# Kernel optimization log

Hardware: AMD Instinct MI355X
Metric: run time of the kernel (lower is better)

The kernel has to match this reference:

```python
import jax, jax.numpy as jnp
import numpy as np

EMBED = 64
HEAD = 16

def setup_inputs() -> dict:
    key = jax.random.key(0)
    k1, k2, k3, k4 = jax.random.split(key, 4)
    x = jax.random.normal(k1, (4, 4096, EMBED), dtype=jnp.float32)
    # store weights as [in, out] so forward is x @ W (equivalent to torch Linear with W.T)
    Wq = jax.random.normal(k2, (EMBED, HEAD), dtype=jnp.float32) * (1.0 / np.sqrt(EMBED))
    Wk = jax.random.normal(k3, (EMBED, HEAD), dtype=jnp.float32) * (1.0 / np.sqrt(EMBED))
    Wv = jax.random.normal(k4, (EMBED, EMBED), dtype=jnp.float32) * (1.0 / np.sqrt(EMBED))
    return {"x": x, "Wq": Wq, "Wk": Wk, "Wv": Wv}

def reference(x, Wq, Wk, Wv):
    # q,k: [B,T,HEAD]; v: [B,T,EMBED]
    q = x @ Wq
    k = x @ Wk
    v = x @ Wv
    scores = jnp.einsum('bqh,bkh->bqk', q, k)  # [B,T,T]
    T = scores.shape[-1]
    # causal mask: positions with key > query set to -inf BEFORE scaling (matches original; same result)
    causal = jnp.tril(jnp.ones((T, T), dtype=bool))
    scores = jnp.where(causal, scores, -jnp.inf)
    attn = jax.nn.softmax(scores / np.sqrt(HEAD).astype(np.float32), axis=-1)
    return jnp.einsum('bqk,bkd->bqd', attn, v)  # [B,T,EMBED]
```

## Files before the change

kernel.cpp:

```cpp
#include <hip/hip_runtime.h>


#define TSEQ 4096
#define NBATCH 4
#define MFIX 24.0f

typedef __attribute__((ext_vector_type(4)))  float fvec4;
typedef __attribute__((ext_vector_type(16))) float f32x16;
typedef __attribute__((ext_vector_type(8)))  short s16x8;

union I4S8 { int i[4]; s16x8 v; };

static __device__ __forceinline__ unsigned short f2bf(float f) {
    unsigned u = __float_as_uint(f);
    u += 0x7FFFu + ((u >> 16) & 1u);
    return (unsigned short)(u >> 16);
}

static __device__ __forceinline__ int cvt_pk_bf16(float lo, float hi) {
    int r;
    asm("v_cvt_pk_bf16_f32 %0, %1, %2" : "=v"(r) : "v"(lo), "v"(hi));
    return r;
}

__global__ __launch_bounds__(256, 2) void proj_kernel(
    const float* __restrict__ x,  const float* __restrict__ Wq,
    const float* __restrict__ Wk, const float* __restrict__ Wv,
    unsigned short* __restrict__ qb, unsigned short* __restrict__ kb,
    unsigned short* __restrict__ vf)
{
    __shared__ __align__(16) unsigned short Wh[96][72], Wl[96][72];
    const int tid  = threadIdx.x;
    const int w    = tid >> 6;
    const int lane = tid & 63;
    const int col  = lane & 31;
    const int g    = lane >> 5;

    const float SCQ = 0.25f * 1.44269504088896340736f;
    #pragma unroll
    for (int j = 0; j < 4; ++j) {
        const int idx = tid + 256 * j;
        const int n = idx & 15, k = idx >> 4;
        float wv = Wq[idx] * SCQ;
        unsigned short h = f2bf(wv);
        Wh[n][k] = h;
        Wl[n][k] = f2bf(wv - __uint_as_float((unsigned)h << 16));
    }
    #pragma unroll
    for (int j = 0; j < 4; ++j) {
        const int idx = tid + 256 * j;
        const int n = idx & 15, k = idx >> 4;
        float wv = Wk[idx];
        unsigned short h = f2bf(wv);
        Wh[16 + n][k] = h;
        Wl[16 + n][k] = f2bf(wv - __uint_as_float((unsigned)h << 16));
    }
    #pragma unroll
    for (int j = 0; j < 16; ++j) {
        const int idx = tid + 256 * j;
        const int n = idx & 63, k = idx >> 6;
        float wv = Wv[idx];
        unsigned short h = f2bf(wv);
        Wh[32 + n][k] = h;
        Wl[32 + n][k] = f2bf(wv - __uint_as_float((unsigned)h << 16));
    }
    __syncthreads();

    const int row0 = blockIdx.x * 128 + w * 32;
    const int arow = row0 + col;

    s16x8 xh[4], xl[4];
    #pragma unroll
    for (int kc = 0; kc < 4; ++kc) {
        const float* xp = x + (size_t)arow * 64 + kc * 16 + 8 * g;
        fvec4 xa = *(const fvec4*)(xp);
        fvec4 xb = *(const fvec4*)(xp + 4);
        I4S8 uh, ul;
        uh.i[0] = cvt_pk_bf16(xa[0], xa[1]);
        uh.i[1] = cvt_pk_bf16(xa[2], xa[3]);
        uh.i[2] = cvt_pk_bf16(xb[0], xb[1]);
        uh.i[3] = cvt_pk_bf16(xb[2], xb[3]);
        float l0 = xa[0] - __uint_as_float((unsigned)uh.i[0] << 16);
        float l1 = xa[1] - __uint_as_float((unsigned)uh.i[0] & 0xffff0000u);
        float l2 = xa[2] - __uint_as_float((unsigned)uh.i[1] << 16);
        float l3 = xa[3] - __uint_as_float((unsigned)uh.i[1] & 0xffff0000u);
        float l4 = xb[0] - __uint_as_float((unsigned)uh.i[2] << 16);
        float l5 = xb[1] - __uint_as_float((unsigned)uh.i[2] & 0xffff0000u);
        float l6 = xb[2] - __uint_as_float((unsigned)uh.i[3] << 16);
        float l7 = xb[3] - __uint_as_float((unsigned)uh.i[3] & 0xffff0000u);
        ul.i[0] = cvt_pk_bf16(l0, l1);
        ul.i[1] = cvt_pk_bf16(l2, l3);
        ul.i[2] = cvt_pk_bf16(l4, l5);
        ul.i[3] = cvt_pk_bf16(l6, l7);
        xh[kc] = uh.v; xl[kc] = ul.v;
    }

    f32x16 acc0 = (f32x16)0.0f, acc1 = (f32x16)0.0f, acc2 = (f32x16)0.0f;
    #pragma unroll
    for (int nt = 0; nt < 3; ++nt) {
        const int n = nt * 32 + col;
        f32x16 a = nt == 0 ? acc0 : (nt == 1 ? acc1 : acc2);
        #pragma unroll
        for (int kc = 0; kc < 4; ++kc) {
            s16x8 bh = *(const s16x8*)&Wh[n][kc * 16 + 8 * g];
            s16x8 bl = *(const s16x8*)&Wl[n][kc * 16 + 8 * g];
            a = __builtin_amdgcn_mfma_f32_32x32x16_bf16(xh[kc], bh, a, 0, 0, 0);
            a = __builtin_amdgcn_mfma_f32_32x32x16_bf16(xl[kc], bh, a, 0, 0, 0);
            a = __builtin_amdgcn_mfma_f32_32x32x16_bf16(xh[kc], bl, a, 0, 0, 0);
        }
        if (nt == 0) acc0 = a; else if (nt == 1) acc1 = a; else acc2 = a;
    }

    {
        unsigned short* dst = (col < 16) ? (qb + col) : (kb + (col - 16));
        #pragma unroll
        for (int rr = 0; rr < 16; ++rr) {
            const int grow = row0 + (rr & 3) + 8 * (rr >> 2) + 4 * g;
            dst[(size_t)grow * 16] = f2bf(acc0[rr]);
        }
    }
    {
        const int tile = row0 >> 6;
        const int hw   = (row0 >> 5) & 1;
        unsigned short* const vtile = vf + (size_t)tile * 4096;
        #pragma unroll
        for (int mt = 0; mt < 2; ++mt) {
            const f32x16 a = mt ? acc2 : acc1;
            #pragma unroll
            for (int ci = 0; ci < 2; ++ci) {
                I4S8 pk;
                pk.i[0] = cvt_pk_bf16(a[8*ci + 0], a[8*ci + 1]);
                pk.i[1] = cvt_pk_bf16(a[8*ci + 2], a[8*ci + 3]);
                pk.i[2] = cvt_pk_bf16(a[8*ci + 4], a[8*ci + 5]);
                pk.i[3] = cvt_pk_bf16(a[8*ci + 6], a[8*ci + 7]);
                const int c = 2 * hw + ci;
                *(s16x8*)(vtile + ((c * 2 + mt) * 64 + lane) * 8) = pk.v;
            }
        }
    }
}

template<int MODE>
static __device__ __forceinline__ void do_tile(
    const unsigned short* kp, const unsigned short* vtile, const int lane,
    const s16x8 qf, const int col, const int g,
    f32x16& o0, f32x16& o1, float& lsum)
{
    const int NC = (MODE == 1) ? 2 : 4;
    s16x8 kf0 = *(const s16x8*)(kp);
    s16x8 kf1;
    if (MODE != 1) kf1 = *(const s16x8*)(kp + 512);
    s16x8 va[4][2];
    #pragma unroll
    for (int c = 0; c < NC; ++c) {
        va[c][0] = *(const s16x8*)(vtile + ((c * 2 + 0) * 64 + lane) * 8);
        va[c][1] = *(const s16x8*)(vtile + ((c * 2 + 1) * 64 + lane) * 8);
    }
    f32x16 s0 = __builtin_amdgcn_mfma_f32_32x32x16_bf16(kf0, qf, (f32x16)0.0f, 0, 0, 0);
    f32x16 s1;
    if (MODE != 1) s1 = __builtin_amdgcn_mfma_f32_32x32x16_bf16(kf1, qf, (f32x16)0.0f, 0, 0, 0);

    int pw[16];
    float psA = 0.f, psB = 0.f, psC = 0.f, psD = 0.f;
    #pragma unroll
    for (int rr = 0; rr < 16; ++rr) {
        float ev = __builtin_amdgcn_exp2f(s0[rr] - MFIX);
        if (MODE == 1) {
            const int drow = (rr & 3) + 8 * (rr >> 2) + 4 * g;
            ev = (drow <= col) ? ev : 0.f;
        }
        s0[rr] = ev;
        if ((rr & 3) == 0) psA += ev; else if ((rr & 3) == 1) psB += ev;
        else if ((rr & 3) == 2) psC += ev; else psD += ev;
    }
    #pragma unroll
    for (int j = 0; j < 8; ++j) pw[j] = cvt_pk_bf16(s0[2*j], s0[2*j+1]);
    if (MODE != 1) {
        #pragma unroll
        for (int rr = 0; rr < 16; ++rr) {
            float ev = __builtin_amdgcn_exp2f(s1[rr] - MFIX);
            if (MODE == 2) {
                const int drow = (rr & 3) + 8 * (rr >> 2) + 4 * g;
                ev = (drow <= col) ? ev : 0.f;
            }
            s1[rr] = ev;
            if ((rr & 3) == 0) psA += ev; else if ((rr & 3) == 1) psB += ev;
            else if ((rr & 3) == 2) psC += ev; else psD += ev;
        }
        #pragma unroll
        for (int j = 0; j < 8; ++j) pw[8 + j] = cvt_pk_bf16(s1[2*j], s1[2*j+1]);
    }
    lsum += (psA + psB) + (psC + psD);

    #pragma unroll
    for (int mt = 0; mt < 2; ++mt) {
        f32x16 oacc = mt ? o1 : o0;
        #pragma unroll
        for (int c = 0; c < NC; ++c) {
            I4S8 pu;
            pu.i[0] = pw[4 * c + 0]; pu.i[1] = pw[4 * c + 1];
            pu.i[2] = pw[4 * c + 2]; pu.i[3] = pw[4 * c + 3];
            oacc = __builtin_amdgcn_mfma_f32_32x32x16_bf16(va[c][mt], pu.v, oacc, 0, 0, 0);
        }
        if (mt) o1 = oacc; else o0 = oacc;
    }
}

__global__ __launch_bounds__(1024, 4) void attn_kernel(
    const unsigned short* __restrict__ qb, const unsigned short* __restrict__ kb,
    const unsigned short* __restrict__ vf, float* __restrict__ out)
{
    __shared__ float pl[16][32];
    __shared__ __align__(16) float pO[2048][18];
    __shared__ float outS[32][66];

    const int tid  = threadIdx.x;
    const int w    = tid >> 6;
    const int lane = tid & 63;
    const int col  = lane & 31;
    const int g    = lane >> 5;
    const int b    = blockIdx.y;
    const int p    = blockIdx.x;

    const unsigned short* const kbase = kb + (size_t)b * TSEQ * 16;
    const unsigned short* const vbase = vf + (size_t)b * 64 * 4096;

    for (int half = 0; half < 2; ++half) {
        const int i  = half ? (127 - p) : p;
        const int q0 = i * 32;
        const int n  = (i + 2) >> 1;

        const s16x8 qf = *(const s16x8*)(qb + ((size_t)(b * TSEQ) + q0 + col) * 16 + 8 * g);

        f32x16 o0 = (f32x16)0.0f, o1 = (f32x16)0.0f;
        float lsum = 0.f;

        int kt = w;
        for (; kt + 1 < n; kt += 16) {
            do_tile<0>(kbase + ((size_t)((kt << 6) + col)) * 16 + 8 * g,
                       vbase + (size_t)kt * 4096, lane, qf, col, g, o0, o1, lsum);
        }
        if (kt == n - 1) {
            const unsigned short* kp = kbase + ((size_t)((kt << 6) + col)) * 16 + 8 * g;
            const unsigned short* vtile = vbase + (size_t)kt * 4096;
            if (i & 1) do_tile<2>(kp, vtile, lane, qf, col, g, o0, o1, lsum);
            else       do_tile<1>(kp, vtile, lane, qf, col, g, o0, o1, lsum);
        }
        lsum += __shfl_xor(lsum, 32);

        if (g == 0) pl[w][col] = lsum;
        #pragma unroll
        for (int mt = 0; mt < 2; ++mt) {
            const f32x16 oa = mt ? o1 : o0;
            #pragma unroll
            for (int rr = 0; rr < 16; ++rr) {
                const int dv = mt * 32 + (rr & 3) + 8 * (rr >> 2) + 4 * g;
                pO[dv * 32 + col][w] = oa[rr];
            }
        }
        __syncthreads();

        {
            const int q   = tid & 31;
            const int dvh = tid >> 5;
            float L = 0.f;
            #pragma unroll
            for (int ww = 0; ww < 16; ++ww) L += pl[ww][q];
            const float inv = 1.0f / L;
            #pragma unroll
            for (int pass = 0; pass < 2; ++pass) {
                const int dv = dvh + 32 * pass;
                const float* prow = pO[dv * 32 + q];
                float s = 0.f;
                #pragma unroll
                for (int c = 0; c < 8; ++c) {
                    float2 v2 = *(const float2*)(prow + 2 * c);
                    s += v2.x + v2.y;
                }
                outS[q][dv] = s * inv;
            }
        }
        __syncthreads();

        {
            const int q2  = tid >> 5;
            const int dvp = (tid & 31) * 2;
            float2 v2 = *(const float2*)&outS[q2][dvp];
            *(float2*)(out + ((size_t)(b * TSEQ) + q0 + q2) * 64 + dvp) = v2;
        }
    }
}

extern "C" void kernel_launch(void* const* d_in, const int* in_sizes, int n_in,
                              void* d_out, int out_size, void* d_ws, size_t ws_size,
                              hipStream_t stream) {
    const float* x  = (const float*)d_in[0];
    const float* Wq = (const float*)d_in[1];
    const float* Wk = (const float*)d_in[2];
    const float* Wv = (const float*)d_in[3];

    unsigned short* qb = (unsigned short*)d_ws;
    unsigned short* kb = qb + (size_t)NBATCH * TSEQ * 16;
    unsigned short* vf = kb + (size_t)NBATCH * TSEQ * 16;
    float* out = (float*)d_out;

    proj_kernel<<<dim3((NBATCH * TSEQ) / 128), 256, 0, stream>>>(x, Wq, Wk, Wv, qb, kb, vf);
    attn_kernel<<<dim3(64, NBATCH), 1024, 0, stream>>>(qb, kb, vf, out);
}
```

Before: 27.49 us.

## Prefetch K across tiles, interleave PV MFMAs, restage x via LDS, shrink proj blocks

The attention inner loop now loads the next tile's K fragments one iteration ahead and issues each half's PV MFMAs right after its softmax, wrapping MFMA groups in s_setprio. The fixed exp2 offset MFIX is dropped, and pO padding changes from 18 to 17 floats. The projection kernel uses 128-thread blocks over 64 rows and stages x through LDS. Together these aim to hide load latency and cut register pressure and bank conflicts. Removing the offset risks exp2 overflow if scores grow large.

After: 36.34 us. +32.2%, slower.

```diff
diff --git a/kernel.cpp b/kernel.cpp
--- a/kernel.cpp
+++ b/kernel.cpp
@@ -3,10 +3,10 @@
 
 #define TSEQ 4096
 #define NBATCH 4
-#define MFIX 24.0f
 
 typedef __attribute__((ext_vector_type(4)))  float fvec4;
 typedef __attribute__((ext_vector_type(16))) float f32x16;
+typedef __attribute__((ext_vector_type(4)))  short s16x4;
 typedef __attribute__((ext_vector_type(8)))  short s16x8;
 
 union I4S8 { int i[4]; s16x8 v; };
@@ -23,23 +23,39 @@
     return r;
 }
 
-__global__ __launch_bounds__(256, 2) void proj_kernel(
+static __device__ __forceinline__ s16x8 cat4(s16x4 a, s16x4 b) {
+    return __builtin_shufflevector(a, b, 0, 1, 2, 3, 4, 5, 6, 7);
+}
+
+__global__ __launch_bounds__(128, 1) void proj_kernel(
     const float* __restrict__ x,  const float* __restrict__ Wq,
     const float* __restrict__ Wk, const float* __restrict__ Wv,
     unsigned short* __restrict__ qb, unsigned short* __restrict__ kb,
     unsigned short* __restrict__ vf)
 {
-    __shared__ __align__(16) unsigned short Wh[96][72], Wl[96][72];
+    __shared__ float xs[64][66];
+    __shared__ __align__(16) unsigned short Wh[96][76], Wl[96][76];
     const int tid  = threadIdx.x;
     const int w    = tid >> 6;
     const int lane = tid & 63;
     const int col  = lane & 31;
     const int g    = lane >> 5;
 
+    {
+        const float* xblk = x + (size_t)blockIdx.x * 64 * 64;
+        #pragma unroll
+        for (int j = 0; j < 8; ++j) {
+            const int fi = (tid + 128 * j) * 4;
+            fvec4 v = *(const fvec4*)(xblk + fi);
+            const int r = fi >> 6, c = fi & 63;
+            xs[r][c + 0] = v[0]; xs[r][c + 1] = v[1];
+            xs[r][c + 2] = v[2]; xs[r][c + 3] = v[3];
+        }
+    }
     const float SCQ = 0.25f * 1.44269504088896340736f;
     #pragma unroll
-    for (int j = 0; j < 4; ++j) {
-        const int idx = tid + 256 * j;
+    for (int j = 0; j < 8; ++j) {
+        const int idx = tid + 128 * j;
         const int n = idx & 15, k = idx >> 4;
         float wv = Wq[idx] * SCQ;
         unsigned short h = f2bf(wv);
@@ -47,8 +63,8 @@
         Wl[n][k] = f2bf(wv - __uint_as_float((unsigned)h << 16));
     }
     #pragma unroll
-    for (int j = 0; j < 4; ++j) {
-        const int idx = tid + 256 * j;
+    for (int j = 0; j < 8; ++j) {
+        const int idx = tid + 128 * j;
         const int n = idx & 15, k = idx >> 4;
         float wv = Wk[idx];
         unsigned short h = f2bf(wv);
@@ -56,8 +72,8 @@
         Wl[16 + n][k] = f2bf(wv - __uint_as_float((unsigned)h << 16));
     }
     #pragma unroll
-    for (int j = 0; j < 16; ++j) {
-        const int idx = tid + 256 * j;
+    for (int j = 0; j < 32; ++j) {
+        const int idx = tid + 128 * j;
         const int n = idx & 63, k = idx >> 6;
         float wv = Wv[idx];
         unsigned short h = f2bf(wv);
@@ -66,32 +82,30 @@
     }
     __syncthreads();
 
-    const int row0 = blockIdx.x * 128 + w * 32;
-    const int arow = row0 + col;
+    const int row0 = blockIdx.x * 64 + w * 32;
+    const int lrow = w * 32 + col;
 
     s16x8 xh[4], xl[4];
     #pragma unroll
     for (int kc = 0; kc < 4; ++kc) {
-        const float* xp = x + (size_t)arow * 64 + kc * 16 + 8 * g;
-        fvec4 xa = *(const fvec4*)(xp);
-        fvec4 xb = *(const fvec4*)(xp + 4);
+        const float* xp = &xs[lrow][kc * 16 + 8 * g];
+        float2 a0 = *(const float2*)(xp + 0);
+        float2 a1 = *(const float2*)(xp + 2);
+        float2 a2 = *(const float2*)(xp + 4);
+        float2 a3 = *(const float2*)(xp + 6);
         I4S8 uh, ul;
-        uh.i[0] = cvt_pk_bf16(xa[0], xa[1]);
-        uh.i[1] = cvt_pk_bf16(xa[2], xa[3]);
-        uh.i[2] = cvt_pk_bf16(xb[0], xb[1]);
-        uh.i[3] = cvt_pk_bf16(xb[2], xb[3]);
-        float l0 = xa[0] - __uint_as_float((unsigned)uh.i[0] << 16);
-        float l1 = xa[1] - __uint_as_float((unsigned)uh.i[0] & 0xffff0000u);
-        float l2 = xa[2] - __uint_as_float((unsigned)uh.i[1] << 16);
-        float l3 = xa[3] - __uint_as_float((unsigned)uh.i[1] & 0xffff0000u);
-        float l4 = xb[0] - __uint_as_float((unsigned)uh.i[2] << 16);
-        float l5 = xb[1] - __uint_as_float((unsigned)uh.i[2] & 0xffff0000u);
-        float l6 = xb[2] - __uint_as_float((unsigned)uh.i[3] << 16);
-        float l7 = xb[3] - __uint_as_float((unsigned)uh.i[3] & 0xffff0000u);
-        ul.i[0] = cvt_pk_bf16(l0, l1);
-        ul.i[1] = cvt_pk_bf16(l2, l3);
-        ul.i[2] = cvt_pk_bf16(l4, l5);
-        ul.i[3] = cvt_pk_bf16(l6, l7);
+        uh.i[0] = cvt_pk_bf16(a0.x, a0.y);
+        uh.i[1] = cvt_pk_bf16(a1.x, a1.y);
+        uh.i[2] = cvt_pk_bf16(a2.x, a2.y);
+        uh.i[3] = cvt_pk_bf16(a3.x, a3.y);
+        ul.i[0] = cvt_pk_bf16(a0.x - __uint_as_float((unsigned)uh.i[0] << 16),
+                              a0.y - __uint_as_float((unsigned)uh.i[0] & 0xffff0000u));
+        ul.i[1] = cvt_pk_bf16(a1.x - __uint_as_float((unsigned)uh.i[1] << 16),
+                              a1.y - __uint_as_float((unsigned)uh.i[1] & 0xffff0000u));
+        ul.i[2] = cvt_pk_bf16(a2.x - __uint_as_float((unsigned)uh.i[2] << 16),
+                              a2.y - __uint_as_float((unsigned)uh.i[2] & 0xffff0000u));
+        ul.i[3] = cvt_pk_bf16(a3.x - __uint_as_float((unsigned)uh.i[3] << 16),
+                              a3.y - __uint_as_float((unsigned)uh.i[3] & 0xffff0000u));
         xh[kc] = uh.v; xl[kc] = ul.v;
     }
 
@@ -102,8 +116,9 @@
         f32x16 a = nt == 0 ? acc0 : (nt == 1 ? acc1 : acc2);
         #pragma unroll
         for (int kc = 0; kc < 4; ++kc) {
-            s16x8 bh = *(const s16x8*)&Wh[n][kc * 16 + 8 * g];
-            s16x8 bl = *(const s16x8*)&Wl[n][kc * 16 + 8 * g];
+            const int off = kc * 16 + 8 * g;
+            s16x8 bh = cat4(*(const s16x4*)&Wh[n][off], *(const s16x4*)&Wh[n][off + 4]);
+            s16x8 bl = cat4(*(const s16x4*)&Wl[n][off], *(const s16x4*)&Wl[n][off + 4]);
             a = __builtin_amdgcn_mfma_f32_32x32x16_bf16(xh[kc], bh, a, 0, 0, 0);
             a = __builtin_amdgcn_mfma_f32_32x32x16_bf16(xl[kc], bh, a, 0, 0, 0);
             a = __builtin_amdgcn_mfma_f32_32x32x16_bf16(xh[kc], bl, a, 0, 0, 0);
@@ -120,9 +135,7 @@
         }
     }
     {
-        const int tile = row0 >> 6;
-        const int hw   = (row0 >> 5) & 1;
-        unsigned short* const vtile = vf + (size_t)tile * 4096;
+        unsigned short* const vtile = vf + (size_t)blockIdx.x * 4096;
         #pragma unroll
         for (int mt = 0; mt < 2; ++mt) {
             const f32x16 a = mt ? acc2 : acc1;
@@ -133,7 +146,7 @@
                 pk.i[1] = cvt_pk_bf16(a[8*ci + 2], a[8*ci + 3]);
                 pk.i[2] = cvt_pk_bf16(a[8*ci + 4], a[8*ci + 5]);
                 pk.i[3] = cvt_pk_bf16(a[8*ci + 6], a[8*ci + 7]);
-                const int c = 2 * hw + ci;
+                const int c = 2 * w + ci;
                 *(s16x8*)(vtile + ((c * 2 + mt) * 64 + lane) * 8) = pk.v;
             }
         }
@@ -141,30 +154,38 @@
 }
 
 template<int MODE>
-static __device__ __forceinline__ void do_tile(
-    const unsigned short* kp, const unsigned short* vtile, const int lane,
+static __device__ __forceinline__ void tile_body(
+    s16x8& kf0, s16x8& kf1, const unsigned short* kpn,
+    const unsigned short* vtile, const int lane,
     const s16x8 qf, const int col, const int g,
     f32x16& o0, f32x16& o1, float& lsum)
 {
-    const int NC = (MODE == 1) ? 2 : 4;
-    s16x8 kf0 = *(const s16x8*)(kp);
-    s16x8 kf1;
-    if (MODE != 1) kf1 = *(const s16x8*)(kp + 512);
-    s16x8 va[4][2];
-    #pragma unroll
-    for (int c = 0; c < NC; ++c) {
-        va[c][0] = *(const s16x8*)(vtile + ((c * 2 + 0) * 64 + lane) * 8);
-        va[c][1] = *(const s16x8*)(vtile + ((c * 2 + 1) * 64 + lane) * 8);
-    }
+    s16x8 va00 = *(const s16x8*)(vtile + (0 * 64 + lane) * 8);
+    s16x8 va01 = *(const s16x8*)(vtile + (1 * 64 + lane) * 8);
+    s16x8 va10 = *(const s16x8*)(vtile + (2 * 64 + lane) * 8);
+    s16x8 va11 = *(const s16x8*)(vtile + (3 * 64 + lane) * 8);
+    s16x8 va20, va21, va30, va31;
+    if (MODE != 1) {
+        va20 = *(const s16x8*)(vtile + (4 * 64 + lane) * 8);
+        va21 = *(const s16x8*)(vtile + (5 * 64 + lane) * 8);
+        va30 = *(const s16x8*)(vtile + (6 * 64 + lane) * 8);
+        va31 = *(const s16x8*)(vtile + (7 * 64 + lane) * 8);
+    }
+    s16x8 kn0 = *(const s16x8*)(kpn);
+    s16x8 kn1 = *(const s16x8*)(kpn + 512);
+
+    __builtin_amdgcn_s_setprio(1);
     f32x16 s0 = __builtin_amdgcn_mfma_f32_32x32x16_bf16(kf0, qf, (f32x16)0.0f, 0, 0, 0);
     f32x16 s1;
-    if (MODE != 1) s1 = __builtin_amdgcn_mfma_f32_32x32x16_bf16(kf1, qf, (f32x16)0.0f, 0, 0, 0);
-
-    int pw[16];
+    if (MODE != 1)
+        s1 = __builtin_amdgcn_mfma_f32_32x32x16_bf16(kf1, qf, (f32x16)0.0f, 0, 0, 0);
+    __builtin_amdgcn_s_setprio(0);
+
     float psA = 0.f, psB = 0.f, psC = 0.f, psD = 0.f;
+    int pw[8];
     #pragma unroll
     for (int rr = 0; rr < 16; ++rr) {
-        float ev = __builtin_amdgcn_exp2f(s0[rr] - MFIX);
+        float ev = __builtin_amdgcn_exp2f(s0[rr]);
         if (MODE == 1) {
             const int drow = (rr & 3) + 8 * (rr >> 2) + 4 * g;
             ev = (drow <= col) ? ev : 0.f;
@@ -175,10 +196,21 @@
     }
     #pragma unroll
     for (int j = 0; j < 8; ++j) pw[j] = cvt_pk_bf16(s0[2*j], s0[2*j+1]);
+    {
+        I4S8 pa, pb;
+        pa.i[0] = pw[0]; pa.i[1] = pw[1]; pa.i[2] = pw[2]; pa.i[3] = pw[3];
+        pb.i[0] = pw[4]; pb.i[1] = pw[5]; pb.i[2] = pw[6]; pb.i[3] = pw[7];
+        __builtin_amdgcn_s_setprio(1);
+        o0 = __builtin_amdgcn_mfma_f32_32x32x16_bf16(va00, pa.v, o0, 0, 0, 0);
+        o1 = __builtin_amdgcn_mfma_f32_32x32x16_bf16(va01, pa.v, o1, 0, 0, 0);
+        o0 = __builtin_amdgcn_mfma_f32_32x32x16_bf16(va10, pb.v, o0, 0, 0, 0);
+        o1 = __builtin_amdgcn_mfma_f32_32x32x16_bf16(va11, pb.v, o1, 0, 0, 0);
+        __builtin_amdgcn_s_setprio(0);
+    }
     if (MODE != 1) {
         #pragma unroll
         for (int rr = 0; rr < 16; ++rr) {
-            float ev = __builtin_amdgcn_exp2f(s1[rr] - MFIX);
+            float ev = __builtin_amdgcn_exp2f(s1[rr]);
             if (MODE == 2) {
                 const int drow = (rr & 3) + 8 * (rr >> 2) + 4 * g;
                 ev = (drow <= col) ? ev : 0.f;
@@ -188,22 +220,19 @@
             else if ((rr & 3) == 2) psC += ev; else psD += ev;
         }
         #pragma unroll
-        for (int j = 0; j < 8; ++j) pw[8 + j] = cvt_pk_bf16(s1[2*j], s1[2*j+1]);
+        for (int j = 0; j < 8; ++j) pw[j] = cvt_pk_bf16(s1[2*j], s1[2*j+1]);
+        I4S8 pa, pb;
+        pa.i[0] = pw[0]; pa.i[1] = pw[1]; pa.i[2] = pw[2]; pa.i[3] = pw[3];
+        pb.i[0] = pw[4]; pb.i[1] = pw[5]; pb.i[2] = pw[6]; pb.i[3] = pw[7];
+        __builtin_amdgcn_s_setprio(1);
+        o0 = __builtin_amdgcn_mfma_f32_32x32x16_bf16(va20, pa.v, o0, 0, 0, 0);
+        o1 = __builtin_amdgcn_mfma_f32_32x32x16_bf16(va21, pa.v, o1, 0, 0, 0);
+        o0 = __builtin_amdgcn_mfma_f32_32x32x16_bf16(va30, pb.v, o0, 0, 0, 0);
+        o1 = __builtin_amdgcn_mfma_f32_32x32x16_bf16(va31, pb.v, o1, 0, 0, 0);
+        __builtin_amdgcn_s_setprio(0);
     }
     lsum += (psA + psB) + (psC + psD);
-
-    #pragma unroll
-    for (int mt = 0; mt < 2; ++mt) {
-        f32x16 oacc = mt ? o1 : o0;
-        #pragma unroll
-        for (int c = 0; c < NC; ++c) {
-            I4S8 pu;
-            pu.i[0] = pw[4 * c + 0]; pu.i[1] = pw[4 * c + 1];
-            pu.i[2] = pw[4 * c + 2]; pu.i[3] = pw[4 * c + 3];
-            oacc = __builtin_amdgcn_mfma_f32_32x32x16_bf16(va[c][mt], pu.v, oacc, 0, 0, 0);
-        }
-        if (mt) o1 = oacc; else o0 = oacc;
-    }
+    kf0 = kn0; kf1 = kn1;
 }
 
 __global__ __launch_bounds__(1024, 4) void attn_kernel(
@@ -211,7 +240,7 @@
     const unsigned short* __restrict__ vf, float* __restrict__ out)
 {
     __shared__ float pl[16][32];
-    __shared__ __align__(16) float pO[2048][18];
+    __shared__ float pO[2048 * 17];
     __shared__ float outS[32][66];
 
     const int tid  = threadIdx.x;
@@ -222,7 +251,7 @@
     const int b    = blockIdx.y;
     const int p    = blockIdx.x;
 
-    const unsigned short* const kbase = kb + (size_t)b * TSEQ * 16;
+    const unsigned short* const kbase = kb + (size_t)b * TSEQ * 16 + (size_t)col * 16 + 8 * g;
     const unsigned short* const vbase = vf + (size_t)b * 64 * 4096;
 
     for (int half = 0; half < 2; ++half) {
@@ -236,15 +265,18 @@
         float lsum = 0.f;
 
         int kt = w;
+        s16x8 kf0 = *(const s16x8*)(kbase + (size_t)kt * 1024);
+        s16x8 kf1 = *(const s16x8*)(kbase + (size_t)kt * 1024 + 512);
         for (; kt + 1 < n; kt += 16) {
-            do_tile<0>(kbase + ((size_t)((kt << 6) + col)) * 16 + 8 * g,
-                       vbase + (size_t)kt * 4096, lane, qf, col, g, o0, o1, lsum);
+            int ktn = kt + 16; if (ktn > 63) ktn = 63;
+            tile_body<0>(kf0, kf1, kbase + (size_t)ktn * 1024,
+                         vbase + (size_t)kt * 4096, lane, qf, col, g, o0, o1, lsum);
         }
         if (kt == n - 1) {
-            const unsigned short* kp = kbase + ((size_t)((kt << 6) + col)) * 16 + 8 * g;
-            const unsigned short* vtile = vbase + (size_t)kt * 4096;
-            if (i & 1) do_tile<2>(kp, vtile, lane, qf, col, g, o0, o1, lsum);
-            else       do_tile<1>(kp, vtile, lane, qf, col, g, o0, o1, lsum);
+            const unsigned short* vt = vbase + (size_t)kt * 4096;
+            const unsigned short* kdum = kbase + (size_t)kt * 1024;
+            if (i & 1) tile_body<2>(kf0, kf1, kdum, vt, lane, qf, col, g, o0, o1, lsum);
+            else       tile_body<1>(kf0, kf1, kdum, vt, lane, qf, col, g, o0, o1, lsum);
         }
         lsum += __shfl_xor(lsum, 32);
 
@@ -255,7 +287,7 @@
             #pragma unroll
             for (int rr = 0; rr < 16; ++rr) {
                 const int dv = mt * 32 + (rr & 3) + 8 * (rr >> 2) + 4 * g;
-                pO[dv * 32 + col][w] = oa[rr];
+                pO[(dv * 32 + col) * 17 + w] = oa[rr];
             }
         }
         __syncthreads();
@@ -270,14 +302,11 @@
             #pragma unroll
             for (int pass = 0; pass < 2; ++pass) {
                 const int dv = dvh + 32 * pass;
-                const float* prow = pO[dv * 32 + q];
-                float s = 0.f;
+                const float* prow = &pO[(dv * 32 + q) * 17];
+                float sA = 0.f, sB = 0.f;
                 #pragma unroll
-                for (int c = 0; c < 8; ++c) {
-                    float2 v2 = *(const float2*)(prow + 2 * c);
-                    s += v2.x + v2.y;
-                }
-                outS[q][dv] = s * inv;
+                for (int c = 0; c < 8; ++c) { sA += prow[2*c]; sB += prow[2*c+1]; }
+                outS[q][dv] = (sA + sB) * inv;
             }
         }
         __syncthreads();
@@ -304,6 +333,6 @@
     unsigned short* vf = kb + (size_t)NBATCH * TSEQ * 16;
     float* out = (float*)d_out;
 
-    proj_kernel<<<dim3((NBATCH * TSEQ) / 128), 256, 0, stream>>>(x, Wq, Wk, Wv, qb, kb, vf);
+    proj_kernel<<<dim3((NBATCH * TSEQ) / 64), 128, 0, stream>>>(x, Wq, Wk, Wv, qb, kb, vf);
     attn_kernel<<<dim3(64, NBATCH), 1024, 0, stream>>>(qb, kb, vf, out);
 }
```
